# Kernel tuning notes

Measured on AMD Instinct MI355X. Metric: run time of the kernel, lower is better.

## Reference

```python
import jax, jax.numpy as jnp
from jax import lax
import numpy as np

D_MODEL = 1024
D_STATE = 16
D_CONV = 4
EXPAND = 2
D_INNER = EXPAND * D_MODEL  # 2048
BATCH = 4
SEQLEN = 2048


def setup_inputs() -> dict:
    key = jax.random.key(0)
    ks = jax.random.split(key, 8)
    s = 0.02  # small init scale for stability
    f32 = jnp.float32
    return {
        "x": jax.random.normal(ks[0], (BATCH, SEQLEN, D_MODEL), f32),
        # Linear weights stored as (in, out); torch applies x @ W.T with W (out, in) -- same math.
        "W_in": (jax.random.normal(ks[1], (D_MODEL, 2 * D_INNER), f32) * s),
        "conv_w": (jax.random.normal(ks[2], (D_INNER, 1, D_CONV), f32) * s),  # depthwise (O, I/groups=1, K)
        "conv_b": jnp.zeros((D_INNER,), f32),
        "W_xproj": (jax.random.normal(ks[3], (D_INNER, 2 * D_STATE), f32) * s),
        "W_dt": (jax.random.normal(ks[4], (D_INNER, D_INNER), f32) * s),
        "b_dt": jnp.zeros((D_INNER,), f32),
        "A_log": jnp.log(jax.random.uniform(ks[5], (D_INNER, D_STATE), f32, 1e-4, 1.0)),
        "D_param": jnp.ones((D_INNER,), f32),
        "W_out": (jax.random.normal(ks[6], (D_INNER, D_MODEL), f32) * s),
    }


def _mamba_forward(x, W_in, conv_w, conv_b, W_xproj, W_dt, b_dt, A_log, D_param, W_out):
    Bb, L, _ = x.shape
    # in_proj and split into x-branch and gate z
    xz = x @ W_in                      # (B, L, 2*d_inner)
    xc, z = jnp.split(xz, 2, axis=-1)
    # causal depthwise conv1d: torch pads both sides by d_conv-1 then slices [:L] == left-pad only
    xt = xc.transpose(0, 2, 1)         # (B, d_inner, L)
    xconv = lax.conv_general_dilated(
        xt, conv_w, window_strides=(1,), padding=[(D_CONV - 1, 0)],
        feature_group_count=D_INNER, dimension_numbers=("NCH", "OIH", "NCH"))
    xs = jax.nn.silu(xconv.transpose(0, 2, 1) + conv_b[None, None, :])  # (B, L, d_inner)
    # SSM inputs
    delta = jax.nn.softplus(xs @ W_dt + b_dt)          # (B, L, d_inner)
    Bs, Cs = jnp.split(xs @ W_xproj, 2, axis=-1)       # each (B, L, d_state)
    A = -jnp.exp(A_log)                                 # (d_inner, d_state)

    def step(h, inp):
        dt, bv, cv, xv = inp                            # (B,d_inner),(B,d_state),(B,d_state),(B,d_inner)
        dA = 1.0 + A[None] * dt[..., None]              # Euler discretization (B, d_inner, d_state)
        dB = bv[:, None, :] * (xv * dt)[..., None]
        h = h * dA + dB
        y = jnp.einsum("bds,bs->bd", h, cv) + D_param * xv
        return h, y

    inputs = (delta.transpose(1, 0, 2), Bs.transpose(1, 0, 2),
              Cs.transpose(1, 0, 2), xs.transpose(1, 0, 2))
    h0 = jnp.zeros((Bb, D_INNER, D_STATE), x.dtype)
    _, ys = lax.scan(step, h0, inputs)                  # ys: (L, B, d_inner)
    y = ys.transpose(1, 0, 2) * jax.nn.silu(z)          # gated output
    return y @ W_out                                    # (B, L, d_model)


def reference(x, W_in, conv_w, conv_b, W_xproj, W_dt, b_dt, A_log, D_param, W_out):
    return _mamba_forward(x, W_in, conv_w, conv_b, W_xproj, W_dt, b_dt, A_log, D_param, W_out)
```

## Files before the change

### kernel.cpp

```cpp
#include <hip/hip_runtime.h>

#define AS1 __attribute__((address_space(1)))
#define AS3 __attribute__((address_space(3)))

typedef unsigned short u16;
typedef __attribute__((ext_vector_type(8))) __bf16 bf16x8;
typedef __attribute__((ext_vector_type(8))) unsigned short u16x8;
typedef __attribute__((ext_vector_type(4))) float f32x4;

#define BATCH   4
#define SEQLEN  2048
#define DMODEL  1024
#define DINNER  2048
#define DSTATE  16
#define ROWS    (BATCH * SEQLEN)

__device__ __forceinline__ u16 f2bf(float f) {
  union { float f; unsigned u; } v; v.f = f;
  unsigned u = v.u;
  return (u16)((u + 0x7fffu + ((u >> 16) & 1u)) >> 16);
}
__device__ __forceinline__ float bf2f(u16 s) {
  union { unsigned u; float f; } v; v.u = ((unsigned)s) << 16;
  return v.f;
}

__global__ void cast_f32_bf16(const float* __restrict__ in, u16* __restrict__ out, int n4) {
  int i = blockIdx.x * blockDim.x + threadIdx.x;
  if (i >= n4) return;
  float4 v = ((const float4*)in)[i];
  ushort4 o;
  o.x = f2bf(v.x); o.y = f2bf(v.y); o.z = f2bf(v.z); o.w = f2bf(v.w);
  ((ushort4*)out)[i] = o;
}

__global__ void transpose_cast(const float* __restrict__ in, u16* __restrict__ out, int R, int C) {
  __shared__ float tile[32][33];
  int x  = blockIdx.x * 32 + threadIdx.x;
  int y0 = blockIdx.y * 32;
#pragma unroll
  for (int j = 0; j < 32; j += 8)
    tile[threadIdx.y + j][threadIdx.x] = in[(size_t)(y0 + threadIdx.y + j) * C + x];
  __syncthreads();
  int xo  = blockIdx.y * 32 + threadIdx.x;
  int yo0 = blockIdx.x * 32;
#pragma unroll
  for (int j = 0; j < 32; j += 8)
    out[(size_t)(yo0 + threadIdx.y + j) * R + xo] = f2bf(tile[threadIdx.x][threadIdx.y + j]);
}

template<int EPI>
__launch_bounds__(256, 2)
__global__ void gemm_bf16(const u16* __restrict__ A, const u16* __restrict__ Bt,
                          void* __restrict__ outp, const float* __restrict__ bias,
                          int M, int N, int K, int gm) {
  __shared__ u16 ldsA[128 * 32];
  __shared__ u16 ldsB[128 * 32];
  const int nb  = gridDim.x;
  const int bid = blockIdx.x;
  const int swz = (bid & 7) * (nb >> 3) + (bid >> 3);
  const int bm = swz % gm, bn = swz / gm;

  const int t = threadIdx.x;
  const int wave = t >> 6, lane = t & 63;
  const int wm = wave >> 1, wn = wave & 1;
  const int lhi = lane >> 4, llo = lane & 15;
  const size_t bm0 = (size_t)bm * 128, bn0 = (size_t)bn * 128;

  f32x4 acc[4][4] = {};

  for (int k0 = 0; k0 < K; k0 += 32) {
#pragma unroll
    for (int c = 0; c < 2; ++c) {
      int e = (c * 256 + t) * 8;
      int row = e >> 5, col = e & 31;
      const u16* gA = A  + (bm0 + row) * K + (k0 + col);
      const u16* gB = Bt + (bn0 + row) * K + (k0 + col);
      __builtin_amdgcn_global_load_lds((const AS1 void*)gA,
          (AS3 void*)(ldsA + c * 2048 + wave * 512), 16, 0, 0);
      __builtin_amdgcn_global_load_lds((const AS1 void*)gB,
          (AS3 void*)(ldsB + c * 2048 + wave * 512), 16, 0, 0);
    }
    __syncthreads();

    bf16x8 af[4], bfr[4];
#pragma unroll
    for (int m = 0; m < 4; ++m)
      af[m] = *(const bf16x8*)(const void*)(ldsA + (wm * 64 + m * 16 + llo) * 32 + lhi * 8);
#pragma unroll
    for (int n = 0; n < 4; ++n)
      bfr[n] = *(const bf16x8*)(const void*)(ldsB + (wn * 64 + n * 16 + llo) * 32 + lhi * 8);
#pragma unroll
    for (int m = 0; m < 4; ++m)
#pragma unroll
      for (int n = 0; n < 4; ++n)
        acc[m][n] = __builtin_amdgcn_mfma_f32_16x16x32_bf16(af[m], bfr[n], acc[m][n], 0, 0, 0);
    __syncthreads();
  }

#pragma unroll
  for (int m = 0; m < 4; ++m) {
#pragma unroll
    for (int n = 0; n < 4; ++n) {
      int col = (int)bn0 + wn * 64 + n * 16 + llo;
#pragma unroll
      for (int r = 0; r < 4; ++r) {
        int row = (int)bm0 + wm * 64 + m * 16 + lhi * 4 + r;
        float v = acc[m][n][r];
        size_t idx = (size_t)row * N + col;
        if (EPI == 0) {
          ((u16*)outp)[idx] = f2bf(v);
        } else if (EPI == 1) {
          float xb = v + bias[col];
          ((float*)outp)[idx] = (xb > 20.f) ? xb : log1pf(__expf(xb));
        } else {
          ((float*)outp)[idx] = v;
        }
      }
    }
  }
}

__global__ void conv_silu(const u16* __restrict__ xz, const float* __restrict__ w,
                          const float* __restrict__ cb, u16* __restrict__ xs, int total) {
  int idx = blockIdx.x * 256 + threadIdx.x;
  if (idx >= total) return;
  int d = idx & (DINNER - 1);
  int l = (idx >> 11) & (SEQLEN - 1);
  int b = idx >> 22;
  float4 wv = ((const float4*)w)[d];
  float acc = cb[d];
#pragma unroll
  for (int k = 0; k < 4; ++k) {
    int li = l - 3 + k;
    if (li >= 0) {
      float xv = bf2f(xz[(size_t)(b * SEQLEN + li) * (2 * DINNER) + d]);
      acc = fmaf((&wv.x)[k], xv, acc);
    }
  }
  float s = acc / (1.f + __expf(-acc));
  xs[(size_t)idx] = f2bf(s);
}

__global__ void xproj_kernel(const u16* __restrict__ xs, const float* __restrict__ Wx,
                             float* __restrict__ outp) {
  __shared__ float part[256];
  int row = blockIdx.x;
  int tid = threadIdx.x;
  int c = tid & 31, kp = tid >> 5;
  const u16* xr = xs + (size_t)row * DINNER + kp * 256;
  const float* wp = Wx + (size_t)(kp * 256) * 32 + c;
  float acc = 0.f;
#pragma unroll 4
  for (int kk = 0; kk < 32; ++kk) {
    u16x8 xv = *(const u16x8*)(const void*)(xr + kk * 8);
#pragma unroll
    for (int j = 0; j < 8; ++j)
      acc = fmaf(bf2f(xv[j]), wp[(kk * 8 + j) * 32], acc);
  }
  part[tid] = acc;
  __syncthreads();
  if (tid < 32) {
    float s = 0.f;
#pragma unroll
    for (int p = 0; p < 8; ++p) s += part[p * 32 + tid];
    outp[(size_t)row * 32 + tid] = s;
  }
}

#define SC_NC 32
#define SC_CL (SEQLEN / SC_NC)
#define SC_DG 16

__launch_bounds__(512, 2)
__global__ void scan_chunked(const float* __restrict__ delta, const u16* __restrict__ xs,
                             const float* __restrict__ xproj, const u16* __restrict__ xz,
                             const float* __restrict__ A_log, const float* __restrict__ Dp,
                             u16* __restrict__ yg) {
  __shared__ float cP[SC_NC][SC_DG][DSTATE];
  __shared__ float cH[SC_NC][SC_DG][DSTATE];
  const int tid = threadIdx.x;
  const int dl = tid & 15, ck = tid >> 4;
  const int b = blockIdx.x >> 7, dblk = blockIdx.x & 127;
  const int d = dblk * SC_DG + dl;
  const int r0 = b * SEQLEN + ck * SC_CL;

  float A[DSTATE];
  {
    const f32x4* ap = (const f32x4*)(A_log + (size_t)d * DSTATE);
#pragma unroll
    for (int q = 0; q < 4; ++q) {
      f32x4 a = ap[q];
#pragma unroll
      for (int j = 0; j < 4; ++j) A[q * 4 + j] = -__expf(a[j]);
    }
  }

  float P[DSTATE], Hh[DSTATE];
#pragma unroll
  for (int s = 0; s < DSTATE; ++s) { P[s] = 1.f; Hh[s] = 0.f; }
#pragma unroll 2
  for (int l = 0; l < SC_CL; ++l) {
    size_t row = (size_t)(r0 + l);
    float dt = delta[row * DINNER + d];
    float xv = bf2f(xs[row * DINNER + d]);
    float dtx = dt * xv;
    const f32x4* bp = (const f32x4*)(xproj + row * 32);
    f32x4 Bq[4];
#pragma unroll
    for (int q = 0; q < 4; ++q) Bq[q] = bp[q];
#pragma unroll
    for (int s = 0; s < DSTATE; ++s) {
      float dA = fmaf(A[s], dt, 1.f);
      P[s] *= dA;
      Hh[s] = fmaf(Hh[s], dA, Bq[s >> 2][s & 3] * dtx);
    }
  }
#pragma unroll
  for (int s = 0; s < DSTATE; ++s) { cP[ck][dl][s] = P[s]; cH[ck][dl][s] = Hh[s]; }
  __syncthreads();

  if (tid < SC_DG * DSTATE) {
    int s2 = tid & 15, dd = tid >> 4;
    float h = 0.f;
    for (int c = 0; c < SC_NC; ++c) {
      float p = cP[c][dd][s2], hh = cH[c][dd][s2];
      cP[c][dd][s2] = h;
      h = fmaf(p, h, hh);
    }
  }
  __syncthreads();

  float h[DSTATE];
#pragma unroll
  for (int s = 0; s < DSTATE; ++s) h[s] = cP[ck][dl][s];
  const float Dv = Dp[d];
#pragma unroll 2
  for (int l = 0; l < SC_CL; ++l) {
    size_t row = (size_t)(r0 + l);
    float dt = delta[row * DINNER + d];
    float xv = bf2f(xs[row * DINNER + d]);
    float dtx = dt * xv;
    const f32x4* bp = (const f32x4*)(xproj + row * 32);
    f32x4 Bq[4], Cq[4];
#pragma unroll
    for (int q = 0; q < 4; ++q) { Bq[q] = bp[q]; Cq[q] = bp[q + 4]; }
    float yp = 0.f;
#pragma unroll
    for (int s = 0; s < DSTATE; ++s) {
      float dA = fmaf(A[s], dt, 1.f);
      h[s] = fmaf(h[s], dA, Bq[s >> 2][s & 3] * dtx);
      yp = fmaf(h[s], Cq[s >> 2][s & 3], yp);
    }
    float z = bf2f(xz[row * (2 * DINNER) + DINNER + d]);
    float y = yp + Dv * xv;
    float g = z / (1.f + __expf(-z));
    yg[row * DINNER + d] = f2bf(y * g);
  }
}

extern "C" void kernel_launch(void* const* d_in, const int* in_sizes, int n_in,
                              void* d_out, int out_size, void* d_ws, size_t ws_size,
                              hipStream_t stream) {
  const float* x       = (const float*)d_in[0];
  const float* W_in    = (const float*)d_in[1];
  const float* conv_w  = (const float*)d_in[2];
  const float* conv_b  = (const float*)d_in[3];
  const float* W_xproj = (const float*)d_in[4];
  const float* W_dt    = (const float*)d_in[5];
  const float* b_dt    = (const float*)d_in[6];
  const float* A_log   = (const float*)d_in[7];
  const float* D_param = (const float*)d_in[8];
  const float* W_out   = (const float*)d_in[9];
  float* out = (float*)d_out;

  char* ws = (char*)d_ws;
  const size_t MB = 1ull << 20;
  u16*   x_bf  = (u16*)(ws);
  u16*   WinT  = (u16*)(ws + 16 * MB);
  u16*   WdtT  = (u16*)(ws + 24 * MB);
  u16*   xz_bf = (u16*)(ws + 32 * MB);
  u16*   xs_bf = (u16*)(ws + 96 * MB);
  float* delta = (float*)(ws + 128 * MB);
  float* xpj   = (float*)(ws + 192 * MB);
  u16*   WoutT = (u16*)(ws + 193 * MB);
  u16*   yg    = (u16*)(ws);

  dim3 tb(32, 8);

  cast_f32_bf16<<<(ROWS * DMODEL / 4 + 255) / 256, 256, 0, stream>>>(x, x_bf, ROWS * DMODEL / 4);
  transpose_cast<<<dim3((2 * DINNER) / 32, DMODEL / 32), tb, 0, stream>>>(W_in, WinT, DMODEL, 2 * DINNER);
  transpose_cast<<<dim3(DINNER / 32, DINNER / 32), tb, 0, stream>>>(W_dt, WdtT, DINNER, DINNER);
  transpose_cast<<<dim3(DMODEL / 32, DINNER / 32), tb, 0, stream>>>(W_out, WoutT, DINNER, DMODEL);

  gemm_bf16<0><<<(ROWS / 128) * ((2 * DINNER) / 128), 256, 0, stream>>>(
      x_bf, WinT, xz_bf, nullptr, ROWS, 2 * DINNER, DMODEL, ROWS / 128);

  conv_silu<<<(ROWS * DINNER) / 256, 256, 0, stream>>>(xz_bf, conv_w, conv_b, xs_bf, ROWS * DINNER);

  gemm_bf16<1><<<(ROWS / 128) * (DINNER / 128), 256, 0, stream>>>(
      xs_bf, WdtT, delta, b_dt, ROWS, DINNER, DINNER, ROWS / 128);

  xproj_kernel<<<ROWS, 256, 0, stream>>>(xs_bf, W_xproj, xpj);

  scan_chunked<<<BATCH * (DINNER / SC_DG), 512, 0, stream>>>(
      delta, xs_bf, xpj, xz_bf, A_log, D_param, yg);

  gemm_bf16<2><<<(ROWS / 128) * (DMODEL / 128), 256, 0, stream>>>(
      yg, WoutT, out, nullptr, ROWS, DMODEL, DINNER, ROWS / 128);
}
```

Baseline: 568.1 us.

## Replace GEMM with 256x256 tiled double-buffered kernel using swizzled LDS

```diff
diff --git a/kernel.cpp b/kernel.cpp
--- a/kernel.cpp
+++ b/kernel.cpp
@@ -50,64 +50,106 @@
 }
 
 template<int EPI>
-__launch_bounds__(256, 2)
-__global__ void gemm_bf16(const u16* __restrict__ A, const u16* __restrict__ Bt,
-                          void* __restrict__ outp, const float* __restrict__ bias,
-                          int M, int N, int K, int gm) {
-  __shared__ u16 ldsA[128 * 32];
-  __shared__ u16 ldsB[128 * 32];
+__launch_bounds__(512, 1)
+__global__ void gemm256(const u16* __restrict__ A, const u16* __restrict__ Bt,
+                        void* __restrict__ outp, const float* __restrict__ bias,
+                        int M, int N, int K, int gm) {
+  extern __shared__ u16 lds[];
   const int nb  = gridDim.x;
   const int bid = blockIdx.x;
   const int swz = (bid & 7) * (nb >> 3) + (bid >> 3);
   const int bm = swz % gm, bn = swz / gm;
 
-  const int t = threadIdx.x;
-  const int wave = t >> 6, lane = t & 63;
-  const int wm = wave >> 1, wn = wave & 1;
-  const int lhi = lane >> 4, llo = lane & 15;
-  const size_t bm0 = (size_t)bm * 128, bn0 = (size_t)bn * 128;
-
-  f32x4 acc[4][4] = {};
-
-  for (int k0 = 0; k0 < K; k0 += 32) {
-#pragma unroll
-    for (int c = 0; c < 2; ++c) {
-      int e = (c * 256 + t) * 8;
-      int row = e >> 5, col = e & 31;
-      const u16* gA = A  + (bm0 + row) * K + (k0 + col);
-      const u16* gB = Bt + (bn0 + row) * K + (k0 + col);
-      __builtin_amdgcn_global_load_lds((const AS1 void*)gA,
-          (AS3 void*)(ldsA + c * 2048 + wave * 512), 16, 0, 0);
-      __builtin_amdgcn_global_load_lds((const AS1 void*)gB,
-          (AS3 void*)(ldsB + c * 2048 + wave * 512), 16, 0, 0);
-    }
-    __syncthreads();
-
-    bf16x8 af[4], bfr[4];
-#pragma unroll
-    for (int m = 0; m < 4; ++m)
-      af[m] = *(const bf16x8*)(const void*)(ldsA + (wm * 64 + m * 16 + llo) * 32 + lhi * 8);
-#pragma unroll
-    for (int n = 0; n < 4; ++n)
-      bfr[n] = *(const bf16x8*)(const void*)(ldsB + (wn * 64 + n * 16 + llo) * 32 + lhi * 8);
-#pragma unroll
-    for (int m = 0; m < 4; ++m)
-#pragma unroll
-      for (int n = 0; n < 4; ++n)
-        acc[m][n] = __builtin_amdgcn_mfma_f32_16x16x32_bf16(af[m], bfr[n], acc[m][n], 0, 0, 0);
-    __syncthreads();
-  }
-
-#pragma unroll
-  for (int m = 0; m < 4; ++m) {
+  const int tid  = threadIdx.x;
+  const int wave = tid >> 6, lane = tid & 63;
+  const int wm = wave >> 2, wn = wave & 3;
+  const int llo = lane & 15, lhi = lane >> 4;
+  const size_t bm0 = (size_t)bm * 256, bn0 = (size_t)bn * 256;
+  const int NT = K >> 6;
+
+  const u16* gA[4]; const u16* gB[4];
+#pragma unroll
+  for (int c = 0; c < 4; ++c) {
+    int ch = c * 512 + tid;
+    int row = ch >> 3;
+    int scol = ((ch & 7) ^ (row & 7)) << 3;
+    gA[c] = A  + (bm0 + row) * (size_t)K + scol;
+    gB[c] = Bt + (bn0 + row) * (size_t)K + scol;
+  }
+
+  const int mask = (llo & 7) << 4;
+  const int ko[2] = { ((0 * 64 + lhi * 16) ^ mask) >> 1, ((1 * 64 + lhi * 16) ^ mask) >> 1 };
+
+#define STAGE(t, bsel)                                                              \
+  do {                                                                              \
+    int k0_ = (t) << 6;                                                             \
+    u16* la_ = lds + (bsel) * 32768;                                                \
+    u16* lb_ = la_ + 16384;                                                         \
+    _Pragma("unroll")                                                               \
+    for (int c = 0; c < 4; ++c)                                                     \
+      __builtin_amdgcn_global_load_lds((const AS1 void*)(gA[c] + k0_),              \
+          (AS3 void*)(la_ + c * 4096 + wave * 512), 16, 0, 0);                      \
+    _Pragma("unroll")                                                               \
+    for (int c = 0; c < 4; ++c)                                                     \
+      __builtin_amdgcn_global_load_lds((const AS1 void*)(gB[c] + k0_),              \
+          (AS3 void*)(lb_ + c * 4096 + wave * 512), 16, 0, 0);                      \
+  } while (0)
+
+  f32x4 acc[8][4] = {};
+
+  STAGE(0, 0);
+  STAGE(1, 1);
+  asm volatile("s_waitcnt vmcnt(8)" ::: "memory");
+  __builtin_amdgcn_s_barrier();
+
+  for (int t = 0; t < NT; ++t) {
+    const int cur = t & 1;
+    const u16* la = lds + cur * 32768;
+    const u16* lb = la + 16384;
+    bf16x8 bfr[4];
+#pragma unroll
+    for (int sub = 0; sub < 4; ++sub) {
+      const int kk = sub >> 1, mh = sub & 1;
+      if (mh == 0) {
+#pragma unroll
+        for (int n = 0; n < 4; ++n)
+          bfr[n] = *(const bf16x8*)(const void*)(lb + (wn * 64 + n * 16 + llo) * 64 + ko[kk]);
+      }
+      bf16x8 af[4];
+#pragma unroll
+      for (int m = 0; m < 4; ++m)
+        af[m] = *(const bf16x8*)(const void*)(la + (wm * 128 + mh * 64 + m * 16 + llo) * 64 + ko[kk]);
+      __builtin_amdgcn_s_barrier();
+      __builtin_amdgcn_s_setprio(1);
+#pragma unroll
+      for (int m = 0; m < 4; ++m)
+#pragma unroll
+        for (int n = 0; n < 4; ++n)
+          acc[mh * 4 + m][n] = __builtin_amdgcn_mfma_f32_16x16x32_bf16(af[m], bfr[n], acc[mh * 4 + m][n], 0, 0, 0);
+      __builtin_amdgcn_s_setprio(0);
+      __builtin_amdgcn_s_barrier();
+    }
+    if (t + 2 < NT) {
+      STAGE(t + 2, cur);
+      asm volatile("s_waitcnt vmcnt(8)" ::: "memory");
+    } else {
+      asm volatile("s_waitcnt vmcnt(0)" ::: "memory");
+    }
+    __builtin_amdgcn_s_barrier();
+  }
+#undef STAGE
+
+#pragma unroll
+  for (int am = 0; am < 8; ++am) {
+    const int mh = am >> 2, m = am & 3;
+    const int rowb = (int)bm0 + wm * 128 + mh * 64 + m * 16 + lhi * 4;
 #pragma unroll
     for (int n = 0; n < 4; ++n) {
-      int col = (int)bn0 + wn * 64 + n * 16 + llo;
+      const int col = (int)bn0 + wn * 64 + n * 16 + llo;
 #pragma unroll
       for (int r = 0; r < 4; ++r) {
-        int row = (int)bm0 + wm * 64 + m * 16 + lhi * 4 + r;
-        float v = acc[m][n][r];
-        size_t idx = (size_t)row * N + col;
+        float v = acc[am][n][r];
+        size_t idx = (size_t)(rowb + r) * N + col;
         if (EPI == 0) {
           ((u16*)outp)[idx] = f2bf(v);
         } else if (EPI == 1) {
@@ -286,6 +328,10 @@
   u16*   WoutT = (u16*)(ws + 193 * MB);
   u16*   yg    = (u16*)(ws);
 
+  hipFuncSetAttribute((const void*)gemm256<0>, hipFuncAttributeMaxDynamicSharedMemorySize, 131072);
+  hipFuncSetAttribute((const void*)gemm256<1>, hipFuncAttributeMaxDynamicSharedMemorySize, 131072);
+  hipFuncSetAttribute((const void*)gemm256<2>, hipFuncAttributeMaxDynamicSharedMemorySize, 131072);
+
   dim3 tb(32, 8);
 
   cast_f32_bf16<<<(ROWS * DMODEL / 4 + 255) / 256, 256, 0, stream>>>(x, x_bf, ROWS * DMODEL / 4);
@@ -293,19 +339,19 @@
   transpose_cast<<<dim3(DINNER / 32, DINNER / 32), tb, 0, stream>>>(W_dt, WdtT, DINNER, DINNER);
   transpose_cast<<<dim3(DMODEL / 32, DINNER / 32), tb, 0, stream>>>(W_out, WoutT, DINNER, DMODEL);
 
-  gemm_bf16<0><<<(ROWS / 128) * ((2 * DINNER) / 128), 256, 0, stream>>>(
-      x_bf, WinT, xz_bf, nullptr, ROWS, 2 * DINNER, DMODEL, ROWS / 128);
+  gemm256<0><<<(ROWS / 256) * ((2 * DINNER) / 256), 512, 131072, stream>>>(
+      x_bf, WinT, xz_bf, nullptr, ROWS, 2 * DINNER, DMODEL, ROWS / 256);
 
   conv_silu<<<(ROWS * DINNER) / 256, 256, 0, stream>>>(xz_bf, conv_w, conv_b, xs_bf, ROWS * DINNER);
 
-  gemm_bf16<1><<<(ROWS / 128) * (DINNER / 128), 256, 0, stream>>>(
-      xs_bf, WdtT, delta, b_dt, ROWS, DINNER, DINNER, ROWS / 128);
+  gemm256<1><<<(ROWS / 256) * (DINNER / 256), 512, 131072, stream>>>(
+      xs_bf, WdtT, delta, b_dt, ROWS, DINNER, DINNER, ROWS / 256);
 
   xproj_kernel<<<ROWS, 256, 0, stream>>>(xs_bf, W_xproj, xpj);
 
   scan_chunked<<<BATCH * (DINNER / SC_DG), 512, 0, stream>>>(
       delta, xs_bf, xpj, xz_bf, A_log, D_param, yg);
 
-  gemm_bf16<2><<<(ROWS / 128) * (DMODEL / 128), 256, 0, stream>>>(
-      yg, WoutT, out, nullptr, ROWS, DMODEL, DINNER, ROWS / 128);
-}
+  gemm256<2><<<(ROWS / 256) * (DMODEL / 256), 512, 131072, stream>>>(
+      yg, WoutT, out, nullptr, ROWS, DMODEL, DINNER, ROWS / 256);
+}
```

Measured after the change: 561.9 us. Within noise of the previous version (-1.1%).

## Replace GEMM with 256-row double-buffered 8-wave pipelined kernel and bf16 delta

Applied to the files above, without the earlier changes.

```diff
diff --git a/kernel.cpp b/kernel.cpp
--- a/kernel.cpp
+++ b/kernel.cpp
@@ -49,70 +49,139 @@
     out[(size_t)(yo0 + threadIdx.y + j) * R + xo] = f2bf(tile[threadIdx.x][threadIdx.y + j]);
 }
 
-template<int EPI>
-__launch_bounds__(256, 2)
-__global__ void gemm_bf16(const u16* __restrict__ A, const u16* __restrict__ Bt,
-                          void* __restrict__ outp, const float* __restrict__ bias,
-                          int M, int N, int K, int gm) {
-  __shared__ u16 ldsA[128 * 32];
-  __shared__ u16 ldsB[128 * 32];
-  const int nb  = gridDim.x;
-  const int bid = blockIdx.x;
-  const int swz = (bid & 7) * (nb >> 3) + (bid >> 3);
-  const int bm = swz % gm, bn = swz / gm;
-
-  const int t = threadIdx.x;
-  const int wave = t >> 6, lane = t & 63;
-  const int wm = wave >> 1, wn = wave & 1;
-  const int lhi = lane >> 4, llo = lane & 15;
-  const size_t bm0 = (size_t)bm * 128, bn0 = (size_t)bn * 128;
-
-  f32x4 acc[4][4] = {};
-
-  for (int k0 = 0; k0 < K; k0 += 32) {
-#pragma unroll
-    for (int c = 0; c < 2; ++c) {
-      int e = (c * 256 + t) * 8;
-      int row = e >> 5, col = e & 31;
-      const u16* gA = A  + (bm0 + row) * K + (k0 + col);
-      const u16* gB = Bt + (bn0 + row) * K + (k0 + col);
-      __builtin_amdgcn_global_load_lds((const AS1 void*)gA,
-          (AS3 void*)(ldsA + c * 2048 + wave * 512), 16, 0, 0);
-      __builtin_amdgcn_global_load_lds((const AS1 void*)gB,
-          (AS3 void*)(ldsB + c * 2048 + wave * 512), 16, 0, 0);
-    }
-    __syncthreads();
-
-    bf16x8 af[4], bfr[4];
-#pragma unroll
-    for (int m = 0; m < 4; ++m)
-      af[m] = *(const bf16x8*)(const void*)(ldsA + (wm * 64 + m * 16 + llo) * 32 + lhi * 8);
-#pragma unroll
-    for (int n = 0; n < 4; ++n)
-      bfr[n] = *(const bf16x8*)(const void*)(ldsB + (wn * 64 + n * 16 + llo) * 32 + lhi * 8);
-#pragma unroll
-    for (int m = 0; m < 4; ++m)
-#pragma unroll
-      for (int n = 0; n < 4; ++n)
-        acc[m][n] = __builtin_amdgcn_mfma_f32_16x16x32_bf16(af[m], bfr[n], acc[m][n], 0, 0, 0);
-    __syncthreads();
-  }
-
-#pragma unroll
-  for (int m = 0; m < 4; ++m) {
-#pragma unroll
-    for (int n = 0; n < 4; ++n) {
-      int col = (int)bn0 + wn * 64 + n * 16 + llo;
+template<int EPI, int BN_>
+__launch_bounds__(512, 1)
+__global__ void gemm8p(const u16* __restrict__ A, const u16* __restrict__ Bt,
+                       void* __restrict__ outp, const float* __restrict__ bias,
+                       int M, int N, int K, int gn, int rr, int cc) {
+  constexpr int NF   = BN_ / 64;
+  constexpr int BCH  = BN_ / 64;
+  constexpr int ASZ  = 256 * 64;
+  constexpr int BSZ  = BN_ * 64;
+  constexpr int BUFS = ASZ + BSZ;
+  extern __shared__ u16 lds[];
+
+  const int xcd = blockIdx.x & 7, kb = blockIdx.x >> 3;
+  const int tpr = gn / cc;
+  const int bm  = (xcd / tpr) * rr + kb / cc;
+  const int bn  = (xcd % tpr) * cc + kb % cc;
+
+  const int tid  = threadIdx.x;
+  const int wave = tid >> 6, lane = tid & 63;
+  const int wm = wave >> 2, wn = wave & 3;
+  const int llo = lane & 15, lhi = lane >> 4;
+  const size_t bm0 = (size_t)bm * 256, bn0 = (size_t)bn * BN_;
+  const int NT = K >> 6;
+
+  const u16* gA[4];
+#pragma unroll
+  for (int ch = 0; ch < 4; ++ch) {
+    int row  = ch * 64 + (tid >> 3);
+    int scol = ((tid & 7) ^ (row & 7)) << 3;
+    gA[ch] = A + (bm0 + row) * (size_t)K + scol;
+  }
+  const u16* gB[BCH];
+#pragma unroll
+  for (int ch = 0; ch < BCH; ++ch) {
+    int row  = ch * 64 + (tid >> 3);
+    int scol = ((tid & 7) ^ (row & 7)) << 3;
+    gB[ch] = Bt + (bn0 + row) * (size_t)K + scol;
+  }
+
+  const int mask = (llo & 7) << 4;
+  const int ko[2] = { ((0 + lhi * 16) ^ mask) >> 1, ((64 + lhi * 16) ^ mask) >> 1 };
+
+#define SGA(t, bsel, ch) __builtin_amdgcn_global_load_lds(                       \
+    (const AS1 void*)(gA[ch] + ((size_t)(t) << 6)),                              \
+    (AS3 void*)(lds + (bsel) * BUFS + (ch) * 4096 + wave * 512), 16, 0, 0)
+#define SGB(t, bsel, ch) __builtin_amdgcn_global_load_lds(                       \
+    (const AS1 void*)(gB[ch] + ((size_t)(t) << 6)),                              \
+    (AS3 void*)(lds + (bsel) * BUFS + ASZ + (ch) * 4096 + wave * 512), 16, 0, 0)
+
+  f32x4 acc[8][NF] = {};
+  bf16x8 bfr[2][NF];
+
+#define PHASE(la_, lb_, MH, KK, RDB, STG, WC)                                    \
+  {                                                                              \
+    bf16x8 af[4];                                                                \
+    _Pragma("unroll") for (int m = 0; m < 4; ++m)                                \
+      af[m] = *(const bf16x8*)(const void*)((la_) + (wm*128 + MH*64 + m*16 + llo)*64 + ko[KK]); \
+    if (RDB) {                                                                   \
+      _Pragma("unroll") for (int n = 0; n < NF; ++n)                             \
+        bfr[KK][n] = *(const bf16x8*)(const void*)((lb_) + (wn*(16*NF) + n*16 + llo)*64 + ko[KK]); \
+    }                                                                            \
+    STG;                                                                         \
+    __builtin_amdgcn_s_barrier();                                                \
+    __builtin_amdgcn_s_setprio(1);                                               \
+    _Pragma("unroll") for (int m = 0; m < 4; ++m)                                \
+      _Pragma("unroll") for (int n = 0; n < NF; ++n)                             \
+        acc[MH*4+m][n] = __builtin_amdgcn_mfma_f32_16x16x32_bf16(af[m], bfr[KK][n], acc[MH*4+m][n], 0, 0, 0); \
+    __builtin_amdgcn_s_setprio(0);                                               \
+    WC;                                                                          \
+    __builtin_amdgcn_s_barrier();                                                \
+  }
+
+  SGA(0, 0, 0); SGA(0, 0, 2); SGB(0, 0, 0); SGB(0, 0, 1);
+  if (BCH == 4) { SGB(0, 0, 2); SGB(0, 0, 3); }
+  SGA(0, 0, 1); SGA(0, 0, 3);
+  SGA(1, 1, 0); SGA(1, 1, 2); SGB(1, 1, 0); SGB(1, 1, 1);
+  asm volatile("s_waitcnt vmcnt(4)" ::: "memory");
+  __builtin_amdgcn_s_barrier();
+
+  const u16* la0 = lds;            const u16* lb0 = lds + ASZ;
+  const u16* la1 = lds + BUFS;     const u16* lb1 = la1 + ASZ;
+
+  for (int u = 0; u < NT; u += 2) {
+    const int v = u + 1;
+    PHASE(la0, lb0, 0, 0, true,
+          ({ if (BCH == 4) { SGB(v, 1, 2); SGB(v, 1, 3); } else { SGA(v, 1, 1); SGA(v, 1, 3); } }),
+          ((void)0));
+    PHASE(la0, lb0, 0, 1, true,
+          ({ if (BCH == 4) { SGA(v, 1, 1); SGA(v, 1, 3); } }),
+          ((void)0));
+    PHASE(la0, lb0, 1, 0, false,
+          ({ if (u + 2 < NT) { SGA(u + 2, 0, 0); SGA(u + 2, 0, 2); } }),
+          ((void)0));
+    PHASE(la0, lb0, 1, 1, false,
+          ({ if (u + 2 < NT) { SGB(u + 2, 0, 0); SGB(u + 2, 0, 1); } }),
+          ({ if (u + 2 < NT) asm volatile("s_waitcnt vmcnt(4)" ::: "memory");
+             else            asm volatile("s_waitcnt vmcnt(0)" ::: "memory"); }));
+    PHASE(la1, lb1, 0, 0, true,
+          ({ if (u + 2 < NT) { if (BCH == 4) { SGB(u + 2, 0, 2); SGB(u + 2, 0, 3); }
+                               else          { SGA(u + 2, 0, 1); SGA(u + 2, 0, 3); } } }),
+          ((void)0));
+    PHASE(la1, lb1, 0, 1, true,
+          ({ if (u + 2 < NT && BCH == 4) { SGA(u + 2, 0, 1); SGA(u + 2, 0, 3); } }),
+          ((void)0));
+    PHASE(la1, lb1, 1, 0, false,
+          ({ if (v + 2 < NT) { SGA(v + 2, 1, 0); SGA(v + 2, 1, 2); } }),
+          ((void)0));
+    PHASE(la1, lb1, 1, 1, false,
+          ({ if (v + 2 < NT) { SGB(v + 2, 1, 0); SGB(v + 2, 1, 1); } }),
+          ({ if (v + 2 < NT) asm volatile("s_waitcnt vmcnt(4)" ::: "memory");
+             else            asm volatile("s_waitcnt vmcnt(0)" ::: "memory"); }));
+  }
+#undef PHASE
+#undef SGA
+#undef SGB
+
+#pragma unroll
+  for (int am = 0; am < 8; ++am) {
+    const int mh = am >> 2, m = am & 3;
+    const int rowb = (int)bm0 + wm * 128 + mh * 64 + m * 16 + lhi * 4;
+#pragma unroll
+    for (int n = 0; n < NF; ++n) {
+      const int col = (int)bn0 + wn * (16 * NF) + n * 16 + llo;
 #pragma unroll
       for (int r = 0; r < 4; ++r) {
-        int row = (int)bm0 + wm * 64 + m * 16 + lhi * 4 + r;
-        float v = acc[m][n][r];
-        size_t idx = (size_t)row * N + col;
+        float v = acc[am][n][r];
+        size_t idx = (size_t)(rowb + r) * N + col;
         if (EPI == 0) {
           ((u16*)outp)[idx] = f2bf(v);
         } else if (EPI == 1) {
           float xb = v + bias[col];
-          ((float*)outp)[idx] = (xb > 20.f) ? xb : log1pf(__expf(xb));
+          float sp = (xb > 20.f) ? xb : log1pf(__expf(xb));
+          ((u16*)outp)[idx] = f2bf(sp);
         } else {
           ((float*)outp)[idx] = v;
         }
@@ -173,7 +242,7 @@
 #define SC_DG 16
 
 __launch_bounds__(512, 2)
-__global__ void scan_chunked(const float* __restrict__ delta, const u16* __restrict__ xs,
+__global__ void scan_chunked(const u16* __restrict__ delta, const u16* __restrict__ xs,
                              const float* __restrict__ xproj, const u16* __restrict__ xz,
                              const float* __restrict__ A_log, const float* __restrict__ Dp,
                              u16* __restrict__ yg) {
@@ -202,7 +271,7 @@
 #pragma unroll 2
   for (int l = 0; l < SC_CL; ++l) {
     size_t row = (size_t)(r0 + l);
-    float dt = delta[row * DINNER + d];
+    float dt = bf2f(delta[row * DINNER + d]);
     float xv = bf2f(xs[row * DINNER + d]);
     float dtx = dt * xv;
     const f32x4* bp = (const f32x4*)(xproj + row * 32);
@@ -238,7 +307,7 @@
 #pragma unroll 2
   for (int l = 0; l < SC_CL; ++l) {
     size_t row = (size_t)(r0 + l);
-    float dt = delta[row * DINNER + d];
+    float dt = bf2f(delta[row * DINNER + d]);
     float xv = bf2f(xs[row * DINNER + d]);
     float dtx = dt * xv;
     const f32x4* bp = (const f32x4*)(xproj + row * 32);
@@ -281,10 +350,14 @@
   u16*   WdtT  = (u16*)(ws + 24 * MB);
   u16*   xz_bf = (u16*)(ws + 32 * MB);
   u16*   xs_bf = (u16*)(ws + 96 * MB);
-  float* delta = (float*)(ws + 128 * MB);
+  u16*   delta = (u16*)(ws + 128 * MB);
   float* xpj   = (float*)(ws + 192 * MB);
   u16*   WoutT = (u16*)(ws + 193 * MB);
   u16*   yg    = (u16*)(ws);
+
+  hipFuncSetAttribute((const void*)gemm8p<0, 256>, hipFuncAttributeMaxDynamicSharedMemorySize, 131072);
+  hipFuncSetAttribute((const void*)gemm8p<1, 256>, hipFuncAttributeMaxDynamicSharedMemorySize, 131072);
+  hipFuncSetAttribute((const void*)gemm8p<2, 128>, hipFuncAttributeMaxDynamicSharedMemorySize, 98304);
 
   dim3 tb(32, 8);
 
@@ -293,19 +366,19 @@
   transpose_cast<<<dim3(DINNER / 32, DINNER / 32), tb, 0, stream>>>(W_dt, WdtT, DINNER, DINNER);
   transpose_cast<<<dim3(DMODEL / 32, DINNER / 32), tb, 0, stream>>>(W_out, WoutT, DINNER, DMODEL);
 
-  gemm_bf16<0><<<(ROWS / 128) * ((2 * DINNER) / 128), 256, 0, stream>>>(
-      x_bf, WinT, xz_bf, nullptr, ROWS, 2 * DINNER, DMODEL, ROWS / 128);
+  gemm8p<0, 256><<<512, 512, 131072, stream>>>(x_bf, WinT, xz_bf, nullptr,
+                                               ROWS, 2 * DINNER, DMODEL, 16, 8, 8);
 
   conv_silu<<<(ROWS * DINNER) / 256, 256, 0, stream>>>(xz_bf, conv_w, conv_b, xs_bf, ROWS * DINNER);
 
-  gemm_bf16<1><<<(ROWS / 128) * (DINNER / 128), 256, 0, stream>>>(
-      xs_bf, WdtT, delta, b_dt, ROWS, DINNER, DINNER, ROWS / 128);
+  gemm8p<1, 256><<<256, 512, 131072, stream>>>(xs_bf, WdtT, delta, b_dt,
+                                               ROWS, DINNER, DINNER, 8, 4, 8);
 
   xproj_kernel<<<ROWS, 256, 0, stream>>>(xs_bf, W_xproj, xpj);
 
   scan_chunked<<<BATCH * (DINNER / SC_DG), 512, 0, stream>>>(
       delta, xs_bf, xpj, xz_bf, A_log, D_param, yg);
 
-  gemm_bf16<2><<<(ROWS / 128) * (DMODEL / 128), 256, 0, stream>>>(
-      yg, WoutT, out, nullptr, ROWS, DMODEL, DINNER, ROWS / 128);
-}
+  gemm8p<2, 128><<<256, 512, 98304, stream>>>(yg, WoutT, out, nullptr,
+                                              ROWS, DMODEL, DINNER, 8, 4, 8);
+}
```

Measured after the change: 513.0 us. 1.11x faster.
